# Kernel tuning notes

Measured on AMD Instinct MI355X. Metric: run time of the kernel, lower is better.

Reference implementation:

```python
import jax, jax.numpy as jnp
import numpy as np

MAX_LEVEL = 12        # config.tree_level_world
FEAT_LEVELS = 3       # config.tree_level_feat
FEAT_DIM = 8          # config.feature_dim
FEAT_STD = 0.05       # config.feature_std
POLY_ON = True        # config.poly_int_on
N = 1048576           # query points
TABLE = 1048577       # corners per level + 1 dummy (zero) row


def setup_inputs() -> dict:
    key = jax.random.key(0)
    k1, k2, k3 = jax.random.split(key, 3)
    coord = jax.random.uniform(k1, (N, 3), jnp.float32, minval=-1.0, maxval=1.0)
    features = FEAT_STD * jax.random.normal(k2, (FEAT_LEVELS, TABLE, FEAT_DIM), jnp.float32)
    indices = jax.random.randint(k3, (FEAT_LEVELS, N, 8), 0, TABLE)
    return {"coord": coord, "features": features, "indices": indices}


def _interp_weights(x, level, polynomial_on=POLY_ON):
    # x: [N,3] in [-1,1]; mirrors FeatureOctree.interpolat
    coords = (2.0 ** level) * (x * 0.5 + 0.5)
    d = coords - jnp.floor(coords)  # torch.frac (coords >= 0 here)
    if polynomial_on:
        d = 3.0 * d * d - 2.0 * d * d * d
    tx, ty, tz = d[:, 0], d[:, 1], d[:, 2]
    _1tx, _1ty, _1tz = 1.0 - tx, 1.0 - ty, 1.0 - tz
    # corner order: z fastest, then y, then x (p0..p7 as in source)
    w = jnp.stack([
        _1tx * _1ty * _1tz, _1tx * _1ty * tz,
        _1tx * ty * _1tz,  _1tx * ty * tz,
        tx * _1ty * _1tz,  tx * _1ty * tz,
        tx * ty * _1tz,    tx * ty * tz,
    ], axis=-1)  # [N,8]
    return w


def reference(coord, features, indices):
    # set_zero(): dummy last row of every level's table is zero
    features = features.at[:, -1, :].set(0.0)
    out = jnp.zeros((coord.shape[0], features.shape[-1]), coord.dtype)
    for i in range(FEAT_LEVELS):  # small fixed hierarchy loop
        current_level = MAX_LEVEL - i
        feature_level = FEAT_LEVELS - i - 1
        w = _interp_weights(coord, current_level)          # [N,8]
        g = features[feature_level][indices[i]]            # gather -> [N,8,D]
        out = out + jnp.einsum('nc,ncd->nd', w, g)
    return out
```

## Files before the change

kernel.cpp:

```cpp
#include <hip/hip_runtime.h>

#define NPTS      1048576
#define TABLE_SZ  1048577
#define NLEVELS   3
#define FDIM      8

__global__ __launch_bounds__(256) void octree_gather_kernel(
    const float* __restrict__ coord,
    const float* __restrict__ features,
    const int*   __restrict__ indices,
    float*       __restrict__ out)
{
    const int tid    = blockIdx.x * blockDim.x + threadIdx.x;
    const int lane_c = tid & 7;
    const int n      = tid >> 3;

    const float x = coord[3 * n + 0];
    const float y = coord[3 * n + 1];
    const float z = coord[3 * n + 2];

    int idx[NLEVELS];
    #pragma unroll
    for (int i = 0; i < NLEVELS; ++i)
        idx[i] = indices[(size_t)i * (size_t)NPTS * 8 + (size_t)tid];

    float4 ga[NLEVELS], gb[NLEVELS];
    #pragma unroll
    for (int i = 0; i < NLEVELS; ++i) {
        const float* ft = features + (size_t)(NLEVELS - 1 - i) * (size_t)TABLE_SZ * FDIM;
        const float4* gp = reinterpret_cast<const float4*>(ft + (size_t)idx[i] * FDIM);
        ga[i] = gp[0];
        gb[i] = gp[1];
    }

    float w[NLEVELS];
    #pragma unroll
    for (int i = 0; i < NLEVELS; ++i) {
        const float scale = (float)(2048 >> i);
        float cx = fmaf(scale, x, scale);
        float cy = fmaf(scale, y, scale);
        float cz = fmaf(scale, z, scale);
        float dx = cx - floorf(cx);
        float dy = cy - floorf(cy);
        float dz = cz - floorf(cz);
        dx = dx * dx * (3.0f - 2.0f * dx);
        dy = dy * dy * (3.0f - 2.0f * dy);
        dz = dz * dz * (3.0f - 2.0f * dz);
        float wi = ((lane_c & 4) ? dx : 1.0f - dx)
                 * ((lane_c & 2) ? dy : 1.0f - dy)
                 * ((lane_c & 1) ? dz : 1.0f - dz);
        w[i] = (idx[i] == TABLE_SZ - 1) ? 0.0f : wi;
    }

    float acc[FDIM];
    #pragma unroll
    for (int d = 0; d < FDIM; ++d) acc[d] = 0.0f;
    #pragma unroll
    for (int i = 0; i < NLEVELS; ++i) {
        acc[0] = fmaf(w[i], ga[i].x, acc[0]);
        acc[1] = fmaf(w[i], ga[i].y, acc[1]);
        acc[2] = fmaf(w[i], ga[i].z, acc[2]);
        acc[3] = fmaf(w[i], ga[i].w, acc[3]);
        acc[4] = fmaf(w[i], gb[i].x, acc[4]);
        acc[5] = fmaf(w[i], gb[i].y, acc[5]);
        acc[6] = fmaf(w[i], gb[i].z, acc[6]);
        acc[7] = fmaf(w[i], gb[i].w, acc[7]);
    }

    const int b0 = lane_c & 1, b1 = (lane_c >> 1) & 1, b2 = (lane_c >> 2) & 1;

    float s4[4];
    #pragma unroll
    for (int j = 0; j < 4; ++j) {
        float snd  = b0 ? acc[2 * j] : acc[2 * j + 1];
        float got  = __shfl_xor(snd, 1);
        float kept = b0 ? acc[2 * j + 1] : acc[2 * j];
        s4[j] = kept + got;
    }
    float s2[2];
    #pragma unroll
    for (int j = 0; j < 2; ++j) {
        float snd  = b1 ? s4[2 * j] : s4[2 * j + 1];
        float got  = __shfl_xor(snd, 2);
        float kept = b1 ? s4[2 * j + 1] : s4[2 * j];
        s2[j] = kept + got;
    }
    {
        float snd  = b2 ? s2[0] : s2[1];
        float got  = __shfl_xor(snd, 4);
        float kept = b2 ? s2[1] : s2[0];
        float s = kept + got;
        out[(size_t)n * FDIM + lane_c] = s;
    }
}

extern "C" void kernel_launch(void* const* d_in, const int* in_sizes, int n_in,
                              void* d_out, int out_size, void* d_ws, size_t ws_size,
                              hipStream_t stream) {
    const float* coord    = (const float*)d_in[0];
    const float* features = (const float*)d_in[1];
    const int*   indices  = (const int*)d_in[2];
    float*       out      = (float*)d_out;

    const int block = 256;
    const long total_threads = (long)NPTS * 8;
    const int grid  = (int)((total_threads + block - 1) / block);
    octree_gather_kernel<<<grid, block, 0, stream>>>(coord, features, indices, out);
}
```

Before: 449.0 us.

## Split each corner gather across two threads with half-row float4 loads

Doubles the thread count so each (point, corner) pair is handled by two threads, each loading one float4 half of the 8-float feature row. The reduction becomes a plain xor-shuffle butterfly over corners, and one thread per half writes a float4 output. The aim is more memory-level parallelism on the random gathers. In exchange, the coord loads and weight computation are duplicated per half, index loads are duplicated, and the launch has twice as many threads.

```diff
diff --git a/kernel.cpp b/kernel.cpp
--- a/kernel.cpp
+++ b/kernel.cpp
@@ -5,15 +5,16 @@
 #define NLEVELS   3
 #define FDIM      8
 
-__global__ __launch_bounds__(256) void octree_gather_kernel(
+__global__ __launch_bounds__(256) void octree_gather16(
     const float* __restrict__ coord,
     const float* __restrict__ features,
     const int*   __restrict__ indices,
     float*       __restrict__ out)
 {
-    const int tid    = blockIdx.x * blockDim.x + threadIdx.x;
-    const int lane_c = tid & 7;
-    const int n      = tid >> 3;
+    const int tid = blockIdx.x * blockDim.x + threadIdx.x;
+    const int h   = tid & 1;
+    const int c   = (tid >> 1) & 7;
+    const int n   = tid >> 4;
 
     const float x = coord[3 * n + 0];
     const float y = coord[3 * n + 1];
@@ -22,15 +23,13 @@
     int idx[NLEVELS];
     #pragma unroll
     for (int i = 0; i < NLEVELS; ++i)
-        idx[i] = indices[(size_t)i * (size_t)NPTS * 8 + (size_t)tid];
+        idx[i] = indices[(size_t)i * (size_t)NPTS * 8 + (size_t)n * 8 + c];
 
-    float4 ga[NLEVELS], gb[NLEVELS];
+    float4 g[NLEVELS];
     #pragma unroll
     for (int i = 0; i < NLEVELS; ++i) {
         const float* ft = features + (size_t)(NLEVELS - 1 - i) * (size_t)TABLE_SZ * FDIM;
-        const float4* gp = reinterpret_cast<const float4*>(ft + (size_t)idx[i] * FDIM);
-        ga[i] = gp[0];
-        gb[i] = gp[1];
+        g[i] = *reinterpret_cast<const float4*>(ft + (size_t)idx[i] * FDIM + h * 4);
     }
 
     float w[NLEVELS];
@@ -46,51 +45,31 @@
         dx = dx * dx * (3.0f - 2.0f * dx);
         dy = dy * dy * (3.0f - 2.0f * dy);
         dz = dz * dz * (3.0f - 2.0f * dz);
-        float wi = ((lane_c & 4) ? dx : 1.0f - dx)
-                 * ((lane_c & 2) ? dy : 1.0f - dy)
-                 * ((lane_c & 1) ? dz : 1.0f - dz);
+        float wi = ((c & 4) ? dx : 1.0f - dx)
+                 * ((c & 2) ? dy : 1.0f - dy)
+                 * ((c & 1) ? dz : 1.0f - dz);
         w[i] = (idx[i] == TABLE_SZ - 1) ? 0.0f : wi;
     }
 
-    float acc[FDIM];
-    #pragma unroll
-    for (int d = 0; d < FDIM; ++d) acc[d] = 0.0f;
+    float4 acc = make_float4(0.f, 0.f, 0.f, 0.f);
     #pragma unroll
     for (int i = 0; i < NLEVELS; ++i) {
-        acc[0] = fmaf(w[i], ga[i].x, acc[0]);
-        acc[1] = fmaf(w[i], ga[i].y, acc[1]);
-        acc[2] = fmaf(w[i], ga[i].z, acc[2]);
-        acc[3] = fmaf(w[i], ga[i].w, acc[3]);
-        acc[4] = fmaf(w[i], gb[i].x, acc[4]);
-        acc[5] = fmaf(w[i], gb[i].y, acc[5]);
-        acc[6] = fmaf(w[i], gb[i].z, acc[6]);
-        acc[7] = fmaf(w[i], gb[i].w, acc[7]);
+        acc.x = fmaf(w[i], g[i].x, acc.x);
+        acc.y = fmaf(w[i], g[i].y, acc.y);
+        acc.z = fmaf(w[i], g[i].z, acc.z);
+        acc.w = fmaf(w[i], g[i].w, acc.w);
     }
 
-    const int b0 = lane_c & 1, b1 = (lane_c >> 1) & 1, b2 = (lane_c >> 2) & 1;
+    #pragma unroll
+    for (int m = 2; m <= 8; m <<= 1) {
+        acc.x += __shfl_xor(acc.x, m);
+        acc.y += __shfl_xor(acc.y, m);
+        acc.z += __shfl_xor(acc.z, m);
+        acc.w += __shfl_xor(acc.w, m);
+    }
 
-    float s4[4];
-    #pragma unroll
-    for (int j = 0; j < 4; ++j) {
-        float snd  = b0 ? acc[2 * j] : acc[2 * j + 1];
-        float got  = __shfl_xor(snd, 1);
-        float kept = b0 ? acc[2 * j + 1] : acc[2 * j];
-        s4[j] = kept + got;
-    }
-    float s2[2];
-    #pragma unroll
-    for (int j = 0; j < 2; ++j) {
-        float snd  = b1 ? s4[2 * j] : s4[2 * j + 1];
-        float got  = __shfl_xor(snd, 2);
-        float kept = b1 ? s4[2 * j + 1] : s4[2 * j];
-        s2[j] = kept + got;
-    }
-    {
-        float snd  = b2 ? s2[0] : s2[1];
-        float got  = __shfl_xor(snd, 4);
-        float kept = b2 ? s2[1] : s2[0];
-        float s = kept + got;
-        out[(size_t)n * FDIM + lane_c] = s;
+    if (c == 0) {
+        *reinterpret_cast<float4*>(out + (size_t)n * FDIM + h * 4) = acc;
     }
 }
 
@@ -103,7 +82,7 @@
     float*       out      = (float*)d_out;
 
     const int block = 256;
-    const long total_threads = (long)NPTS * 8;
+    const long total_threads = (long)NPTS * 16;
     const int grid  = (int)((total_threads + block - 1) / block);
-    octree_gather_kernel<<<grid, block, 0, stream>>>(coord, features, indices, out);
+    octree_gather16<<<grid, block, 0, stream>>>(coord, features, indices, out);
 }
```

New measurement: 467.1 us. 1.04x slower.

## Convert gather kernel to persistent grid with software-prefetched indices and coords

Applied to the files above, without the earlier changes.

Replaces the one-thread-per-corner launch with a fixed grid of 2048 blocks that loops over points in grid-stride sweeps. Each iteration prefetches the next sweep's indices and coordinates while it gathers and reduces the current one. This aims to hide index-load latency behind the dependent feature gathers and cut block launch overhead. The risk is that the fixed grid limits in-flight memory parallelism compared with the large original grid, and the extra registers may lower occupancy.

```diff
diff --git a/kernel.cpp b/kernel.cpp
--- a/kernel.cpp
+++ b/kernel.cpp
@@ -5,92 +5,114 @@
 #define NLEVELS   3
 #define FDIM      8
 
-__global__ __launch_bounds__(256) void octree_gather_kernel(
+#define NBLOCKS 2048
+#define PTS_PER_SWEEP ((NBLOCKS * 256) / 8)
+#define NITER (NPTS / PTS_PER_SWEEP)
+
+__global__ __launch_bounds__(256, 8) void octree_persistent(
     const float* __restrict__ coord,
     const float* __restrict__ features,
     const int*   __restrict__ indices,
     float*       __restrict__ out)
 {
-    const int tid    = blockIdx.x * blockDim.x + threadIdx.x;
-    const int lane_c = tid & 7;
-    const int n      = tid >> 3;
+    const int tid = blockIdx.x * blockDim.x + threadIdx.x;
+    const int c   = tid & 7;
+    int p = tid >> 3;
 
-    const float x = coord[3 * n + 0];
-    const float y = coord[3 * n + 1];
-    const float z = coord[3 * n + 2];
-
-    int idx[NLEVELS];
+    int   idx_c[NLEVELS];
+    float cx_c, cy_c, cz_c;
     #pragma unroll
     for (int i = 0; i < NLEVELS; ++i)
-        idx[i] = indices[(size_t)i * (size_t)NPTS * 8 + (size_t)tid];
+        idx_c[i] = indices[(size_t)i * (size_t)NPTS * 8 + (size_t)p * 8 + c];
+    cx_c = coord[3 * p + 0];
+    cy_c = coord[3 * p + 1];
+    cz_c = coord[3 * p + 2];
 
-    float4 ga[NLEVELS], gb[NLEVELS];
-    #pragma unroll
-    for (int i = 0; i < NLEVELS; ++i) {
-        const float* ft = features + (size_t)(NLEVELS - 1 - i) * (size_t)TABLE_SZ * FDIM;
-        const float4* gp = reinterpret_cast<const float4*>(ft + (size_t)idx[i] * FDIM);
-        ga[i] = gp[0];
-        gb[i] = gp[1];
-    }
+    for (int it = 0; it < NITER; ++it) {
+        float4 ga[NLEVELS], gb[NLEVELS];
+        #pragma unroll
+        for (int i = 0; i < NLEVELS; ++i) {
+            const float* ft = features + (size_t)(NLEVELS - 1 - i) * (size_t)TABLE_SZ * FDIM;
+            const float4* gp = reinterpret_cast<const float4*>(ft + (size_t)idx_c[i] * FDIM);
+            ga[i] = gp[0];
+            gb[i] = gp[1];
+        }
 
-    float w[NLEVELS];
-    #pragma unroll
-    for (int i = 0; i < NLEVELS; ++i) {
-        const float scale = (float)(2048 >> i);
-        float cx = fmaf(scale, x, scale);
-        float cy = fmaf(scale, y, scale);
-        float cz = fmaf(scale, z, scale);
-        float dx = cx - floorf(cx);
-        float dy = cy - floorf(cy);
-        float dz = cz - floorf(cz);
-        dx = dx * dx * (3.0f - 2.0f * dx);
-        dy = dy * dy * (3.0f - 2.0f * dy);
-        dz = dz * dz * (3.0f - 2.0f * dz);
-        float wi = ((lane_c & 4) ? dx : 1.0f - dx)
-                 * ((lane_c & 2) ? dy : 1.0f - dy)
-                 * ((lane_c & 1) ? dz : 1.0f - dz);
-        w[i] = (idx[i] == TABLE_SZ - 1) ? 0.0f : wi;
-    }
+        const int pn = p + PTS_PER_SWEEP;
+        int   idx_n[NLEVELS];
+        float cx_n = 0.f, cy_n = 0.f, cz_n = 0.f;
+        if (it + 1 < NITER) {
+            #pragma unroll
+            for (int i = 0; i < NLEVELS; ++i)
+                idx_n[i] = indices[(size_t)i * (size_t)NPTS * 8 + (size_t)pn * 8 + c];
+            cx_n = coord[3 * pn + 0];
+            cy_n = coord[3 * pn + 1];
+            cz_n = coord[3 * pn + 2];
+        } else {
+            #pragma unroll
+            for (int i = 0; i < NLEVELS; ++i) idx_n[i] = 0;
+        }
 
-    float acc[FDIM];
-    #pragma unroll
-    for (int d = 0; d < FDIM; ++d) acc[d] = 0.0f;
-    #pragma unroll
-    for (int i = 0; i < NLEVELS; ++i) {
-        acc[0] = fmaf(w[i], ga[i].x, acc[0]);
-        acc[1] = fmaf(w[i], ga[i].y, acc[1]);
-        acc[2] = fmaf(w[i], ga[i].z, acc[2]);
-        acc[3] = fmaf(w[i], ga[i].w, acc[3]);
-        acc[4] = fmaf(w[i], gb[i].x, acc[4]);
-        acc[5] = fmaf(w[i], gb[i].y, acc[5]);
-        acc[6] = fmaf(w[i], gb[i].z, acc[6]);
-        acc[7] = fmaf(w[i], gb[i].w, acc[7]);
-    }
+        float w[NLEVELS];
+        #pragma unroll
+        for (int i = 0; i < NLEVELS; ++i) {
+            const float scale = (float)(2048 >> i);
+            float fx = fmaf(scale, cx_c, scale);
+            float fy = fmaf(scale, cy_c, scale);
+            float fz = fmaf(scale, cz_c, scale);
+            float dx = fx - floorf(fx);
+            float dy = fy - floorf(fy);
+            float dz = fz - floorf(fz);
+            dx = dx * dx * (3.0f - 2.0f * dx);
+            dy = dy * dy * (3.0f - 2.0f * dy);
+            dz = dz * dz * (3.0f - 2.0f * dz);
+            float wi = ((c & 4) ? dx : 1.0f - dx)
+                     * ((c & 2) ? dy : 1.0f - dy)
+                     * ((c & 1) ? dz : 1.0f - dz);
+            w[i] = (idx_c[i] == TABLE_SZ - 1) ? 0.0f : wi;
+        }
 
-    const int b0 = lane_c & 1, b1 = (lane_c >> 1) & 1, b2 = (lane_c >> 2) & 1;
+        float acc[FDIM];
+        #pragma unroll
+        for (int d = 0; d < FDIM; ++d) acc[d] = 0.0f;
+        #pragma unroll
+        for (int i = 0; i < NLEVELS; ++i) {
+            acc[0] = fmaf(w[i], ga[i].x, acc[0]);
+            acc[1] = fmaf(w[i], ga[i].y, acc[1]);
+            acc[2] = fmaf(w[i], ga[i].z, acc[2]);
+            acc[3] = fmaf(w[i], ga[i].w, acc[3]);
+            acc[4] = fmaf(w[i], gb[i].x, acc[4]);
+            acc[5] = fmaf(w[i], gb[i].y, acc[5]);
+            acc[6] = fmaf(w[i], gb[i].z, acc[6]);
+            acc[7] = fmaf(w[i], gb[i].w, acc[7]);
+        }
 
-    float s4[4];
-    #pragma unroll
-    for (int j = 0; j < 4; ++j) {
-        float snd  = b0 ? acc[2 * j] : acc[2 * j + 1];
-        float got  = __shfl_xor(snd, 1);
-        float kept = b0 ? acc[2 * j + 1] : acc[2 * j];
-        s4[j] = kept + got;
-    }
-    float s2[2];
-    #pragma unroll
-    for (int j = 0; j < 2; ++j) {
-        float snd  = b1 ? s4[2 * j] : s4[2 * j + 1];
-        float got  = __shfl_xor(snd, 2);
-        float kept = b1 ? s4[2 * j + 1] : s4[2 * j];
-        s2[j] = kept + got;
-    }
-    {
+        const int b0 = c & 1, b1 = (c >> 1) & 1, b2 = (c >> 2) & 1;
+        float s4[4];
+        #pragma unroll
+        for (int j = 0; j < 4; ++j) {
+            float snd  = b0 ? acc[2 * j] : acc[2 * j + 1];
+            float got  = __shfl_xor(snd, 1);
+            float kept = b0 ? acc[2 * j + 1] : acc[2 * j];
+            s4[j] = kept + got;
+        }
+        float s2[2];
+        #pragma unroll
+        for (int j = 0; j < 2; ++j) {
+            float snd  = b1 ? s4[2 * j] : s4[2 * j + 1];
+            float got  = __shfl_xor(snd, 2);
+            float kept = b1 ? s4[2 * j + 1] : s4[2 * j];
+            s2[j] = kept + got;
+        }
         float snd  = b2 ? s2[0] : s2[1];
         float got  = __shfl_xor(snd, 4);
         float kept = b2 ? s2[1] : s2[0];
-        float s = kept + got;
-        out[(size_t)n * FDIM + lane_c] = s;
+        out[(size_t)p * FDIM + c] = kept + got;
+
+        p = pn;
+        #pragma unroll
+        for (int i = 0; i < NLEVELS; ++i) idx_c[i] = idx_n[i];
+        cx_c = cx_n; cy_c = cy_n; cz_c = cz_n;
     }
 }
 
@@ -102,8 +124,5 @@
     const int*   indices  = (const int*)d_in[2];
     float*       out      = (float*)d_out;
 
-    const int block = 256;
-    const long total_threads = (long)NPTS * 8;
-    const int grid  = (int)((total_threads + block - 1) / block);
-    octree_gather_kernel<<<grid, block, 0, stream>>>(coord, features, indices, out);
+    octree_persistent<<<NBLOCKS, 256, 0, stream>>>(coord, features, indices, out);
 }
```

After: 474.4 us. 5.6% more time.
